# Kernel optimization log

Measured on AMD Instinct MI355X. Metric: run time of the kernel, lower is better.

The kernel has to match this reference:

```python
import jax, jax.numpy as jnp
import numpy as np

NUM_GRAPHS = 64
BN_EPS = 1e-5


def setup_inputs() -> dict:
    key = jax.random.key(0)
    ks = jax.random.split(key, 20)
    N, E, D, H, C, L = 100_000, 1_600_000, 128, 128, 16, 4
    x = jax.random.normal(ks[0], (N, D), jnp.float32)
    edge_index = jax.random.randint(ks[1], (2, E), 0, N, jnp.int32)
    batch = jnp.sort(jax.random.randint(ks[2], (N,), 0, NUM_GRAPHS, jnp.int32))
    s = 0.05
    conv_W = jax.random.normal(ks[3], (L, D, H), jnp.float32) * s
    conv_b = jnp.zeros((L, H), jnp.float32)
    bn_gamma = jnp.ones((L, H), jnp.float32)
    bn_beta = jnp.zeros((L, H), jnp.float32)
    bn_mean = jax.random.normal(ks[4], (L, H), jnp.float32) * 0.01
    bn_var = jnp.ones((L, H), jnp.float32)
    cls_W1 = jax.random.normal(ks[5], (H, H), jnp.float32) * s
    cls_b1 = jnp.zeros((H,), jnp.float32)
    cls_W2 = jax.random.normal(ks[6], (H, C), jnp.float32) * s
    cls_b2 = jnp.zeros((C,), jnp.float32)
    nov_W1 = jax.random.normal(ks[7], (H, H), jnp.float32) * s
    nov_b1 = jnp.zeros((H,), jnp.float32)
    nov_W2 = jax.random.normal(ks[8], (H, 1), jnp.float32) * s
    nov_b2 = jnp.zeros((1,), jnp.float32)
    return {
        'x': x, 'edge_index': edge_index, 'batch': batch,
        'conv_W': conv_W, 'conv_b': conv_b,
        'bn_gamma': bn_gamma, 'bn_beta': bn_beta, 'bn_mean': bn_mean, 'bn_var': bn_var,
        'cls_W1': cls_W1, 'cls_b1': cls_b1, 'cls_W2': cls_W2, 'cls_b2': cls_b2,
        'nov_W1': nov_W1, 'nov_b1': nov_b1, 'nov_W2': nov_W2, 'nov_b2': nov_b2,
    }


def reference(x, edge_index, batch, conv_W, conv_b, bn_gamma, bn_beta, bn_mean, bn_var,
              cls_W1, cls_b1, cls_W2, cls_b2, nov_W1, nov_b1, nov_W2, nov_b2):
    N = x.shape[0]
    src, dst = edge_index[0], edge_index[1]
    # symmetric GCN normalization with self-loops: deg = in-degree + 1
    deg = jax.ops.segment_sum(jnp.ones(src.shape[0], x.dtype), dst, num_segments=N) + 1.0
    dis = jax.lax.rsqrt(deg)  # [N]
    edge_norm = (dis[src] * dis[dst])[:, None]  # [E,1]
    self_norm = (dis * dis)[:, None]            # [N,1]

    h = x
    for l in range(conv_W.shape[0]):
        hw = h @ conv_W[l]                                   # [N,H]
        agg = jax.ops.segment_sum(hw[src] * edge_norm, dst, num_segments=N)
        hw = agg + hw * self_norm + conv_b[l]                # GCNConv output
        # BatchNorm1d, eval mode (running stats); dropout is identity in eval
        hw = (hw - bn_mean[l]) * (bn_gamma[l] / jnp.sqrt(bn_var[l] + BN_EPS)) + bn_beta[l]
        h = jax.nn.relu(hw)

    pooled = jax.ops.segment_sum(h, batch, num_segments=NUM_GRAPHS)  # global_add_pool [G,H]
    logits = jax.nn.relu(pooled @ cls_W1 + cls_b1) @ cls_W2 + cls_b2           # [G,C]
    novelty = jax.nn.sigmoid(jax.nn.relu(pooled @ nov_W1 + nov_b1) @ nov_W2 + nov_b2)  # [G,1]
    return (logits, novelty)
```

## Files before the change

### kernel.cpp

```cpp
#include <hip/hip_runtime.h>
#include <hip/hip_fp16.h>
#include <cstdint>
#include <cstddef>

#define NUM_GRAPHS 64
#define HDIM 128
#define NBLK_S 256

typedef __attribute__((ext_vector_type(8))) _Float16 half8v;
typedef __attribute__((ext_vector_type(4))) float float4v;

__global__ __launch_bounds__(256) void count_hist_kernel(const int* __restrict__ dst,
                                                         int* __restrict__ cnt,
                                                         int* __restrict__ hist,
                                                         int E, int chunk, int shift, int NB) {
    __shared__ int lh[256];
    int t = threadIdx.x;
    int b = blockIdx.x;
    lh[t] = 0;
    __syncthreads();
    int beg = b * chunk;
    int end = beg + chunk; if (end > E) end = E;
    for (int i = beg + t; i < end; i += 256) {
        int d = dst[i];
        atomicAdd(&cnt[d], 1);
        atomicAdd(&lh[d >> shift], 1);
    }
    __syncthreads();
    for (int k = t; k < NB; k += 256) hist[k * NBLK_S + b] = lh[k];
}

__global__ __launch_bounds__(256) void scan_partial_kernel(const int* __restrict__ in,
                                                           int* __restrict__ blockSums, int M) {
    __shared__ int s[256];
    int t = threadIdx.x;
    int base = blockIdx.x * 4096 + t * 16;
    int local = 0;
#pragma unroll
    for (int i = 0; i < 16; ++i) {
        int idx = base + i;
        if (idx < M) local += in[idx];
    }
    s[t] = local;
    __syncthreads();
    for (int off = 128; off > 0; off >>= 1) {
        if (t < off) s[t] += s[t + off];
        __syncthreads();
    }
    if (t == 0) blockSums[blockIdx.x] = s[0];
}

__global__ __launch_bounds__(1024) void scan_blocksums_kernel(int* __restrict__ blockSums,
                                                              int* __restrict__ row_ptr_or_null,
                                                              int nb, int E, int N) {
    __shared__ int s[1024];
    int t = threadIdx.x;
    int v = (t < nb) ? blockSums[t] : 0;
    s[t] = v;
    __syncthreads();
    for (int off = 1; off < 1024; off <<= 1) {
        int u = (t >= off) ? s[t - off] : 0;
        __syncthreads();
        s[t] += u;
        __syncthreads();
    }
    if (t < nb) blockSums[t] = s[t] - v;
    if (t == 0 && row_ptr_or_null) row_ptr_or_null[N] = E;
}

__global__ __launch_bounds__(256) void scan_apply_kernel(const int* __restrict__ cnt,
                                                         const int* __restrict__ blockSums,
                                                         int* __restrict__ row_ptr,
                                                         int* __restrict__ fill,
                                                         float* __restrict__ dis, int N) {
    __shared__ int s[256];
    int t = threadIdx.x;
    int base = blockIdx.x * 4096 + t * 16;
    int c[16];
    int local = 0;
#pragma unroll
    for (int i = 0; i < 16; ++i) {
        int idx = base + i;
        c[i] = (idx < N) ? cnt[idx] : 0;
        local += c[i];
    }
    s[t] = local;
    __syncthreads();
    for (int off = 1; off < 256; off <<= 1) {
        int u = (t >= off) ? s[t - off] : 0;
        __syncthreads();
        s[t] += u;
        __syncthreads();
    }
    int pos = blockSums[blockIdx.x] + s[t] - local;
#pragma unroll
    for (int i = 0; i < 16; ++i) {
        int idx = base + i;
        if (idx < N) {
            row_ptr[idx] = pos;
            fill[idx] = pos;
            dis[idx] = rsqrtf((float)c[i] + 1.0f);
            pos += c[i];
        }
    }
}

__global__ __launch_bounds__(256) void scan_apply_generic(int* __restrict__ io,
                                                          const int* __restrict__ blockSums, int M) {
    __shared__ int s[256];
    int t = threadIdx.x;
    int base = blockIdx.x * 4096 + t * 16;
    int c[16];
    int local = 0;
#pragma unroll
    for (int i = 0; i < 16; ++i) {
        int idx = base + i;
        c[i] = (idx < M) ? io[idx] : 0;
        local += c[i];
    }
    s[t] = local;
    __syncthreads();
    for (int off = 1; off < 256; off <<= 1) {
        int u = (t >= off) ? s[t - off] : 0;
        __syncthreads();
        s[t] += u;
        __syncthreads();
    }
    int pos = blockSums[blockIdx.x] + s[t] - local;
#pragma unroll
    for (int i = 0; i < 16; ++i) {
        int idx = base + i;
        if (idx < M) {
            io[idx] = pos;
            pos += c[i];
        }
    }
}

__global__ __launch_bounds__(256) void scatter_bucket_kernel(const int* __restrict__ src,
                                                             const int* __restrict__ dst,
                                                             const int* __restrict__ hist,
                                                             int2* __restrict__ pairs,
                                                             int E, int chunk, int shift, int NB) {
    __shared__ int base[256];
    int t = threadIdx.x;
    int b = blockIdx.x;
    for (int k = t; k < NB; k += 256) base[k] = hist[k * NBLK_S + b];
    __syncthreads();
    int beg = b * chunk;
    int end = beg + chunk; if (end > E) end = E;
    for (int i = beg + t; i < end; i += 256) {
        int d = dst[i];
        int s = src[i];
        int pos = atomicAdd(&base[d >> shift], 1);
        pairs[pos] = make_int2(s, d);
    }
}

__global__ __launch_bounds__(256) void fill_pairs_kernel(const int2* __restrict__ pairs,
                                                         int* __restrict__ fill,
                                                         int* __restrict__ sorted_src, int E) {
    int i = blockIdx.x * 256 + threadIdx.x;
    if (i < E) {
        int2 p = pairs[i];
        int pos = atomicAdd(&fill[p.y], 1);
        sorted_src[pos] = p.x;
    }
}

__global__ __launch_bounds__(256) void fold_kernel(const float* __restrict__ gamma,
                                                   const float* __restrict__ beta,
                                                   const float* __restrict__ mean,
                                                   const float* __restrict__ var,
                                                   const float* __restrict__ convb,
                                                   float* __restrict__ scale,
                                                   float* __restrict__ bias, int LH) {
    int i = blockIdx.x * 256 + threadIdx.x;
    if (i < LH) {
        float gs = gamma[i] * rsqrtf(var[i] + 1e-5f);
        scale[i] = gs;
        bias[i] = (convb[i] - mean[i]) * gs + beta[i];
    }
}

__global__ __launch_bounds__(256) void f32_to_f16_kernel(const float* __restrict__ in,
                                                         __half* __restrict__ out, int n2) {
    int stride = gridDim.x * 256;
    for (int i = blockIdx.x * 256 + threadIdx.x; i < n2; i += stride) {
        float2 v = ((const float2*)in)[i];
        ((__half2*)out)[i] = __floats2half2_rn(v.x, v.y);
    }
}

__global__ __launch_bounds__(64) void pack_W_kernel(const float* __restrict__ W,
                                                    __half* __restrict__ hi,
                                                    __half* __restrict__ lo) {
    int b = blockIdx.x;
    int l = b >> 5;
    int ntile = (b >> 2) & 7;
    int kchunk = b & 3;
    int lane = threadIdx.x;
    int n = ntile * 16 + (lane & 15);
    int kbase = kchunk * 32 + (lane >> 4) * 8;
    size_t ob = ((size_t)b * 64 + lane) * 8;
#pragma unroll
    for (int j = 0; j < 8; ++j) {
        float w = W[(size_t)l * 16384 + (size_t)(kbase + j) * 128 + n];
        __half hb = __float2half_rn(w);
        float rem = w - __half2float(hb);
        hi[ob + j] = hb;
        lo[ob + j] = __float2half_rn(rem);
    }
}

__global__ __launch_bounds__(256) void gemm_mfma_f16(const __half* __restrict__ h,
                                                     const __half* __restrict__ Whi,
                                                     const __half* __restrict__ Wlo,
                                                     const float* __restrict__ dis,
                                                     __half* __restrict__ out, int N) {
    int wave = threadIdx.x >> 6;
    int lane = threadIdx.x & 63;
    int lrow = lane & 15;
    int lk8 = lane >> 4;
    int mbase = blockIdx.x * 128 + wave * 32;

    float4v acc[2][8];
#pragma unroll
    for (int mt = 0; mt < 2; ++mt)
#pragma unroll
        for (int nt = 0; nt < 8; ++nt) {
            acc[mt][nt][0] = 0.f; acc[mt][nt][1] = 0.f;
            acc[mt][nt][2] = 0.f; acc[mt][nt][3] = 0.f;
        }

    const half8v* BH = (const half8v*)Whi;
    const half8v* BL = (const half8v*)Wlo;
    const half8v* H8 = (const half8v*)h;

    for (int kc = 0; kc < 4; ++kc) {
        half8v a[2];
#pragma unroll
        for (int mt = 0; mt < 2; ++mt) {
            int node = mbase + mt * 16 + lrow;
            if (node < N) {
                a[mt] = H8[(size_t)node * 16 + kc * 4 + lk8];
            } else {
#pragma unroll
                for (int j = 0; j < 8; ++j) a[mt][j] = (_Float16)0;
            }
        }
#pragma unroll
        for (int nt = 0; nt < 8; ++nt) {
            half8v bh = BH[(size_t)(nt * 4 + kc) * 64 + lane];
            half8v bl = BL[(size_t)(nt * 4 + kc) * 64 + lane];
#pragma unroll
            for (int mt = 0; mt < 2; ++mt) {
                acc[mt][nt] = __builtin_amdgcn_mfma_f32_16x16x32_f16(a[mt], bh, acc[mt][nt], 0, 0, 0);
                acc[mt][nt] = __builtin_amdgcn_mfma_f32_16x16x32_f16(a[mt], bl, acc[mt][nt], 0, 0, 0);
            }
        }
    }

#pragma unroll
    for (int mt = 0; mt < 2; ++mt) {
#pragma unroll
        for (int r = 0; r < 4; ++r) {
            int node = mbase + mt * 16 + lk8 * 4 + r;
            if (node < N) {
                float dn = dis[node];
#pragma unroll
                for (int nt = 0; nt < 8; ++nt)
                    out[(size_t)node * HDIM + nt * 16 + lrow] = __float2half_rn(acc[mt][nt][r] * dn);
            }
        }
    }
}

__global__ __launch_bounds__(256) void agg_kernel(const __half* __restrict__ hwp,
                                                  const int* __restrict__ row_ptr,
                                                  const int* __restrict__ sorted_src,
                                                  const float* __restrict__ dis,
                                                  const float* __restrict__ scale,
                                                  const float* __restrict__ bias,
                                                  __half* __restrict__ hout, int N) {
    int wave = threadIdx.x >> 6;
    int lane = threadIdx.x & 63;
    int n = blockIdx.x * 4 + wave;
    if (n >= N) return;
    const __half2* hw2 = (const __half2*)hwp;

    float2 acc = __half22float2(hw2[(size_t)n * 64 + lane]);
    int e0 = row_ptr[n];
    int e1 = row_ptr[n + 1];
    int e = e0;
    for (; e + 3 < e1; e += 4) {
        int s0 = sorted_src[e];
        int s1 = sorted_src[e + 1];
        int s2 = sorted_src[e + 2];
        int s3 = sorted_src[e + 3];
        float2 v0 = __half22float2(hw2[(size_t)s0 * 64 + lane]);
        float2 v1 = __half22float2(hw2[(size_t)s1 * 64 + lane]);
        float2 v2 = __half22float2(hw2[(size_t)s2 * 64 + lane]);
        float2 v3 = __half22float2(hw2[(size_t)s3 * 64 + lane]);
        acc.x += v0.x + v1.x + v2.x + v3.x;
        acc.y += v0.y + v1.y + v2.y + v3.y;
    }
    for (; e < e1; ++e) {
        float2 v0 = __half22float2(hw2[(size_t)sorted_src[e] * 64 + lane]);
        acc.x += v0.x;
        acc.y += v0.y;
    }
    float dn = dis[n];
    int f0 = lane * 2;
    float y0 = fmaxf(dn * acc.x * scale[f0] + bias[f0], 0.f);
    float y1 = fmaxf(dn * acc.y * scale[f0 + 1] + bias[f0 + 1], 0.f);
    ((__half2*)hout)[(size_t)n * 64 + lane] = __floats2half2_rn(y0, y1);
}

__global__ __launch_bounds__(128) void pool_kernel(const __half* __restrict__ h,
                                                   const int* __restrict__ batch,
                                                   float* __restrict__ pooled, int N) {
    int f = threadIdx.x;
    int n0 = blockIdx.x * 256;
    if (n0 >= N) return;
    int nend = n0 + 256; if (nend > N) nend = N;
    float acc = 0.f;
    int g = batch[n0];
    for (int n = n0; n < nend; ++n) {
        int gn = batch[n];
        if (gn != g) {
            atomicAdd(&pooled[g * HDIM + f], acc);
            acc = 0.f;
            g = gn;
        }
        acc += __half2float(h[(size_t)n * HDIM + f]);
    }
    atomicAdd(&pooled[g * HDIM + f], acc);
}

__global__ __launch_bounds__(128) void head_kernel(const float* __restrict__ pooled,
                                                   const float* __restrict__ cW1, const float* __restrict__ cb1,
                                                   const float* __restrict__ cW2, const float* __restrict__ cb2,
                                                   const float* __restrict__ nW1, const float* __restrict__ nb1,
                                                   const float* __restrict__ nW2, const float* __restrict__ nb2,
                                                   float* __restrict__ out) {
    __shared__ float p[128];
    __shared__ float hid[128];
    int g = blockIdx.x, t = threadIdx.x;
    p[t] = pooled[g * HDIM + t];
    __syncthreads();

    float a = cb1[t];
    for (int k = 0; k < 128; ++k) a += p[k] * cW1[k * 128 + t];
    hid[t] = fmaxf(a, 0.f);
    __syncthreads();
    if (t < 16) {
        float acc = cb2[t];
        for (int j = 0; j < 128; ++j) acc += hid[j] * cW2[j * 16 + t];
        out[g * 16 + t] = acc;
    }
    __syncthreads();

    float b = nb1[t];
    for (int k = 0; k < 128; ++k) b += p[k] * nW1[k * 128 + t];
    hid[t] = fmaxf(b, 0.f);
    __syncthreads();
    if (t == 0) {
        float acc = nb2[0];
        for (int j = 0; j < 128; ++j) acc += hid[j] * nW2[j];
        out[NUM_GRAPHS * 16 + g] = 1.f / (1.f + expf(-acc));
    }
}

extern "C" void kernel_launch(void* const* d_in, const int* in_sizes, int n_in,
                              void* d_out, int out_size, void* d_ws, size_t ws_size,
                              hipStream_t stream) {
    const float* x       = (const float*)d_in[0];
    const int*   ei      = (const int*)d_in[1];
    const int*   batch   = (const int*)d_in[2];
    const float* conv_W  = (const float*)d_in[3];
    const float* conv_b  = (const float*)d_in[4];
    const float* bn_g    = (const float*)d_in[5];
    const float* bn_b    = (const float*)d_in[6];
    const float* bn_m    = (const float*)d_in[7];
    const float* bn_v    = (const float*)d_in[8];
    const float* cW1     = (const float*)d_in[9];
    const float* cb1     = (const float*)d_in[10];
    const float* cW2     = (const float*)d_in[11];
    const float* cb2     = (const float*)d_in[12];
    const float* nW1     = (const float*)d_in[13];
    const float* nb1     = (const float*)d_in[14];
    const float* nW2     = (const float*)d_in[15];
    const float* nb2     = (const float*)d_in[16];

    const int N = in_sizes[2];
    const int E = in_sizes[1] / 2;
    const int L = in_sizes[3] / (128 * 128);
    const int H = HDIM;

    const int* src = ei;
    const int* dst = ei + E;

    int shift = 9;
    while ((((N - 1) >> shift) + 1) > 256) ++shift;
    const int NB = ((N - 1) >> shift) + 1;
    const int M = NB * NBLK_S;
    const int chunk = (E + NBLK_S - 1) / NBLK_S;

    char* w = (char*)d_ws;
    size_t o = 0;
    auto alloc = [&](size_t bytes) -> void* {
        void* p = w + o;
        o = (o + bytes + 255) & ~(size_t)255;
        return p;
    };
    int nscanN = (N + 4095) / 4096;
    int nscanM = (M + 4095) / 4096;
    int nscanMax = nscanN > nscanM ? nscanN : nscanM;

    int*    cnt        = (int*)alloc((size_t)N * 4);
    int*    fill       = (int*)alloc((size_t)N * 4);
    int*    row_ptr    = (int*)alloc((size_t)(N + 1) * 4);
    float*  dis        = (float*)alloc((size_t)N * 4);
    float*  scale      = (float*)alloc((size_t)L * H * 4);
    float*  bias       = (float*)alloc((size_t)L * H * 4);
    int*    blockSums  = (int*)alloc((size_t)nscanMax * 4);
    int*    hist       = (int*)alloc((size_t)M * 4);
    int2*   pairs      = (int2*)alloc((size_t)E * 8);
    int*    sorted_src = (int*)alloc((size_t)E * 4);
    __half* Whi        = (__half*)alloc((size_t)L * H * H * 2);
    __half* Wlo        = (__half*)alloc((size_t)L * H * H * 2);
    __half* x16        = (__half*)alloc((size_t)N * H * 2);
    __half* bufA       = (__half*)alloc((size_t)N * H * 2);
    __half* bufB       = (__half*)alloc((size_t)N * H * 2);
    float*  pooled     = (float*)alloc((size_t)NUM_GRAPHS * H * 4);

    hipMemsetAsync(cnt, 0, (size_t)N * 4, stream);
    hipMemsetAsync(pooled, 0, (size_t)NUM_GRAPHS * H * 4, stream);

    count_hist_kernel<<<NBLK_S, 256, 0, stream>>>(dst, cnt, hist, E, chunk, shift, NB);
    scan_partial_kernel<<<nscanN, 256, 0, stream>>>(cnt, blockSums, N);
    scan_blocksums_kernel<<<1, 1024, 0, stream>>>(blockSums, row_ptr, nscanN, E, N);
    scan_apply_kernel<<<nscanN, 256, 0, stream>>>(cnt, blockSums, row_ptr, fill, dis, N);
    scan_partial_kernel<<<nscanM, 256, 0, stream>>>(hist, blockSums, M);
    scan_blocksums_kernel<<<1, 1024, 0, stream>>>(blockSums, nullptr, nscanM, 0, 0);
    scan_apply_generic<<<nscanM, 256, 0, stream>>>(hist, blockSums, M);
    scatter_bucket_kernel<<<NBLK_S, 256, 0, stream>>>(src, dst, hist, pairs, E, chunk, shift, NB);
    fill_pairs_kernel<<<(E + 255) / 256, 256, 0, stream>>>(pairs, fill, sorted_src, E);

    fold_kernel<<<(L * H + 255) / 256, 256, 0, stream>>>(bn_g, bn_b, bn_m, bn_v, conv_b,
                                                         scale, bias, L * H);
    pack_W_kernel<<<L * 32, 64, 0, stream>>>(conv_W, Whi, Wlo);
    f32_to_f16_kernel<<<2048, 256, 0, stream>>>(x, x16, N * H / 2);

    const __half* hin = x16;
    for (int l = 0; l < L; ++l) {
        gemm_mfma_f16<<<(N + 127) / 128, 256, 0, stream>>>(hin,
                                                           Whi + (size_t)l * H * H,
                                                           Wlo + (size_t)l * H * H,
                                                           dis, bufA, N);
        agg_kernel<<<(N + 3) / 4, 256, 0, stream>>>(bufA, row_ptr, sorted_src, dis,
                                                    scale + l * H, bias + l * H, bufB, N);
        hin = bufB;
    }

    pool_kernel<<<(N + 255) / 256, 128, 0, stream>>>(bufB, batch, pooled, N);
    head_kernel<<<NUM_GRAPHS, 128, 0, stream>>>(pooled, cW1, cb1, cW2, cb2,
                                                nW1, nb1, nW2, nb2, (float*)d_out);
}
```

Baseline: 774.4 us.

## Fuse input fp32-to-fp16 conversion into first GEMM and widen aggregation gathers

The separate f32-to-f16 conversion kernel is removed; the first-layer GEMM now reads fp32 x directly and converts in registers, saving an intermediate write and read. The aggregation kernel now has each half-wave gather a different neighbor with 8-byte loads (4 halves per lane), processing two edges per wave step and combining via a cross-half shuffle. This raises the number of gathers in flight and cuts the instruction count per edge, at the cost of a reduction shuffle and some idle lanes on odd-degree tails.

```diff
diff --git a/kernel.cpp b/kernel.cpp
--- a/kernel.cpp
+++ b/kernel.cpp
@@ -183,15 +183,6 @@
     }
 }
 
-__global__ __launch_bounds__(256) void f32_to_f16_kernel(const float* __restrict__ in,
-                                                         __half* __restrict__ out, int n2) {
-    int stride = gridDim.x * 256;
-    for (int i = blockIdx.x * 256 + threadIdx.x; i < n2; i += stride) {
-        float2 v = ((const float2*)in)[i];
-        ((__half2*)out)[i] = __floats2half2_rn(v.x, v.y);
-    }
-}
-
 __global__ __launch_bounds__(64) void pack_W_kernel(const float* __restrict__ W,
                                                     __half* __restrict__ hi,
                                                     __half* __restrict__ lo) {
@@ -213,7 +204,8 @@
     }
 }
 
-__global__ __launch_bounds__(256) void gemm_mfma_f16(const __half* __restrict__ h,
+__global__ __launch_bounds__(256) void gemm_mfma_f16(const __half* __restrict__ h16,
+                                                     const float* __restrict__ h32,
                                                      const __half* __restrict__ Whi,
                                                      const __half* __restrict__ Wlo,
                                                      const float* __restrict__ dis,
@@ -235,7 +227,7 @@
 
     const half8v* BH = (const half8v*)Whi;
     const half8v* BL = (const half8v*)Wlo;
-    const half8v* H8 = (const half8v*)h;
+    const half8v* H8 = (const half8v*)h16;
 
     for (int kc = 0; kc < 4; ++kc) {
         half8v a[2];
@@ -243,7 +235,16 @@
         for (int mt = 0; mt < 2; ++mt) {
             int node = mbase + mt * 16 + lrow;
             if (node < N) {
-                a[mt] = H8[(size_t)node * 16 + kc * 4 + lk8];
+                if (h32) {
+                    const float4* hp = (const float4*)&h32[(size_t)node * HDIM + kc * 32 + lk8 * 8];
+                    float4 f0 = hp[0], f1 = hp[1];
+                    a[mt][0] = (_Float16)f0.x; a[mt][1] = (_Float16)f0.y;
+                    a[mt][2] = (_Float16)f0.z; a[mt][3] = (_Float16)f0.w;
+                    a[mt][4] = (_Float16)f1.x; a[mt][5] = (_Float16)f1.y;
+                    a[mt][6] = (_Float16)f1.z; a[mt][7] = (_Float16)f1.w;
+                } else {
+                    a[mt] = H8[(size_t)node * 16 + kc * 4 + lk8];
+                }
             } else {
 #pragma unroll
                 for (int j = 0; j < 8; ++j) a[mt][j] = (_Float16)0;
@@ -276,9 +277,15 @@
     }
 }
 
+__device__ inline void acc_add8(float4& a, uint2 v) {
+    float2 f0 = __half22float2(*(__half2*)&v.x);
+    float2 f1 = __half22float2(*(__half2*)&v.y);
+    a.x += f0.x; a.y += f0.y; a.z += f1.x; a.w += f1.y;
+}
+
 __global__ __launch_bounds__(256) void agg_kernel(const __half* __restrict__ hwp,
                                                   const int* __restrict__ row_ptr,
-                                                  const int* __restrict__ sorted_src,
+                                                  const int* __restrict__ ss,
                                                   const float* __restrict__ dis,
                                                   const float* __restrict__ scale,
                                                   const float* __restrict__ bias,
@@ -287,34 +294,73 @@
     int lane = threadIdx.x & 63;
     int n = blockIdx.x * 4 + wave;
     if (n >= N) return;
-    const __half2* hw2 = (const __half2*)hwp;
-
-    float2 acc = __half22float2(hw2[(size_t)n * 64 + lane]);
+    int hid = lane >> 5;
+    int l32 = lane & 31;
+    const uint2* rows = (const uint2*)hwp;
+
+    float4 acc0 = make_float4(0.f, 0.f, 0.f, 0.f);
+    float4 acc1 = make_float4(0.f, 0.f, 0.f, 0.f);
+
+    if (hid == 0) {
+        uint2 sv = rows[(size_t)n * 32 + l32];
+        acc_add8(acc0, sv);
+    }
+
     int e0 = row_ptr[n];
     int e1 = row_ptr[n + 1];
     int e = e0;
-    for (; e + 3 < e1; e += 4) {
-        int s0 = sorted_src[e];
-        int s1 = sorted_src[e + 1];
-        int s2 = sorted_src[e + 2];
-        int s3 = sorted_src[e + 3];
-        float2 v0 = __half22float2(hw2[(size_t)s0 * 64 + lane]);
-        float2 v1 = __half22float2(hw2[(size_t)s1 * 64 + lane]);
-        float2 v2 = __half22float2(hw2[(size_t)s2 * 64 + lane]);
-        float2 v3 = __half22float2(hw2[(size_t)s3 * 64 + lane]);
-        acc.x += v0.x + v1.x + v2.x + v3.x;
-        acc.y += v0.y + v1.y + v2.y + v3.y;
-    }
-    for (; e < e1; ++e) {
-        float2 v0 = __half22float2(hw2[(size_t)sorted_src[e] * 64 + lane]);
-        acc.x += v0.x;
-        acc.y += v0.y;
-    }
-    float dn = dis[n];
-    int f0 = lane * 2;
-    float y0 = fmaxf(dn * acc.x * scale[f0] + bias[f0], 0.f);
-    float y1 = fmaxf(dn * acc.y * scale[f0 + 1] + bias[f0 + 1], 0.f);
-    ((__half2*)hout)[(size_t)n * 64 + lane] = __floats2half2_rn(y0, y1);
+    for (; e + 7 < e1; e += 8) {
+        int sA = ss[e], sB = ss[e + 1], sC = ss[e + 2], sD = ss[e + 3];
+        int sE = ss[e + 4], sF = ss[e + 5], sG = ss[e + 6], sH = ss[e + 7];
+        int q0 = hid ? sB : sA;
+        int q1 = hid ? sD : sC;
+        int q2 = hid ? sF : sE;
+        int q3 = hid ? sH : sG;
+        uint2 v0 = rows[(size_t)q0 * 32 + l32];
+        uint2 v1 = rows[(size_t)q1 * 32 + l32];
+        uint2 v2 = rows[(size_t)q2 * 32 + l32];
+        uint2 v3 = rows[(size_t)q3 * 32 + l32];
+        acc_add8(acc0, v0);
+        acc_add8(acc1, v1);
+        acc_add8(acc0, v2);
+        acc_add8(acc1, v3);
+    }
+    for (; e + 1 < e1; e += 2) {
+        int sA = ss[e], sB = ss[e + 1];
+        int q0 = hid ? sB : sA;
+        uint2 v0 = rows[(size_t)q0 * 32 + l32];
+        acc_add8(acc0, v0);
+    }
+    if (e < e1) {
+        if (hid == 0) {
+            int sA = ss[e];
+            uint2 v0 = rows[(size_t)sA * 32 + l32];
+            acc_add8(acc1, v0);
+        }
+    }
+    acc0.x += acc1.x; acc0.y += acc1.y; acc0.z += acc1.z; acc0.w += acc1.w;
+
+    acc0.x += __shfl_xor(acc0.x, 32);
+    acc0.y += __shfl_xor(acc0.y, 32);
+    acc0.z += __shfl_xor(acc0.z, 32);
+    acc0.w += __shfl_xor(acc0.w, 32);
+
+    if (hid == 0) {
+        float dn = dis[n];
+        int f0 = l32 * 4;
+        float4 sc = *(const float4*)&scale[f0];
+        float4 bs = *(const float4*)&bias[f0];
+        float y0 = fmaxf(dn * acc0.x * sc.x + bs.x, 0.f);
+        float y1 = fmaxf(dn * acc0.y * sc.y + bs.y, 0.f);
+        float y2 = fmaxf(dn * acc0.z * sc.z + bs.z, 0.f);
+        float y3 = fmaxf(dn * acc0.w * sc.w + bs.w, 0.f);
+        __half2 o0 = __floats2half2_rn(y0, y1);
+        __half2 o1 = __floats2half2_rn(y2, y3);
+        uint2 ov;
+        ov.x = *(unsigned*)&o0;
+        ov.y = *(unsigned*)&o1;
+        ((uint2*)hout)[(size_t)n * 32 + l32] = ov;
+    }
 }
 
 __global__ __launch_bounds__(128) void pool_kernel(const __half* __restrict__ h,
@@ -430,7 +476,6 @@
     int*    sorted_src = (int*)alloc((size_t)E * 4);
     __half* Whi        = (__half*)alloc((size_t)L * H * H * 2);
     __half* Wlo        = (__half*)alloc((size_t)L * H * H * 2);
-    __half* x16        = (__half*)alloc((size_t)N * H * 2);
     __half* bufA       = (__half*)alloc((size_t)N * H * 2);
     __half* bufB       = (__half*)alloc((size_t)N * H * 2);
     float*  pooled     = (float*)alloc((size_t)NUM_GRAPHS * H * 4);
@@ -451,11 +496,10 @@
     fold_kernel<<<(L * H + 255) / 256, 256, 0, stream>>>(bn_g, bn_b, bn_m, bn_v, conv_b,
                                                          scale, bias, L * H);
     pack_W_kernel<<<L * 32, 64, 0, stream>>>(conv_W, Whi, Wlo);
-    f32_to_f16_kernel<<<2048, 256, 0, stream>>>(x, x16, N * H / 2);
-
-    const __half* hin = x16;
+
+    const __half* hin = nullptr;
     for (int l = 0; l < L; ++l) {
-        gemm_mfma_f16<<<(N + 127) / 128, 256, 0, stream>>>(hin,
+        gemm_mfma_f16<<<(N + 127) / 128, 256, 0, stream>>>(hin, l == 0 ? x : nullptr,
                                                            Whi + (size_t)l * H * H,
                                                            Wlo + (size_t)l * H * H,
                                                            dis, bufA, N);
```

New measurement: 745.7 us. 3.7% less time.
